# Kernel optimization log

Measured on AMD Instinct MI355X. Metric: run time of the kernel, lower is better.

Reference implementation:

```python
import jax, jax.numpy as jnp
import numpy as np
import math

B, S, D, H = 4, 1024, 1024, 16
HD = D // H
R = 128  # max_rel_pos
EPS = 1e-5

def setup_inputs() -> dict:
    key = jax.random.key(0)
    ks = jax.random.split(key, 20)
    sd = 1.0 / math.sqrt(D)
    def lin(k, din, dout):
        return jax.random.normal(k, (din, dout), jnp.float32) * (1.0 / math.sqrt(din))
    return {
        "x": jax.random.normal(ks[0], (B, S, D), jnp.float32),
        "wq": lin(ks[1], D, D), "bq": jnp.zeros((D,), jnp.float32),
        "wk": lin(ks[2], D, D), "bk": jnp.zeros((D,), jnp.float32),
        "wv": lin(ks[3], D, D), "bv": jnp.zeros((D,), jnp.float32),
        "wo": lin(ks[4], D, D), "bo": jnp.zeros((D,), jnp.float32),
        "rel_embed": jax.random.normal(ks[5], (2 * R + 1, HD), jnp.float32),
        "ln1_g": jnp.ones((D,), jnp.float32), "ln1_b": jnp.zeros((D,), jnp.float32),
        "ln2_g": jnp.ones((D,), jnp.float32), "ln2_b": jnp.zeros((D,), jnp.float32),
        "w1": lin(ks[6], D, 4 * D), "b1": jnp.zeros((4 * D,), jnp.float32),
        "w2": lin(ks[7], 4 * D, D), "b2": jnp.zeros((D,), jnp.float32),
    }

def _layernorm(x, g, b):
    mu = jnp.mean(x, axis=-1, keepdims=True)
    var = jnp.mean(jnp.square(x - mu), axis=-1, keepdims=True)
    return (x - mu) * jax.lax.rsqrt(var + EPS) * g + b

def _block(x, wq, bq, wk, bk, wv, bv, wo, bo, rel_embed,
           ln1_g, ln1_b, ln2_g, ln2_b, w1, b1, w2, b2):
    h = _layernorm(x, ln1_g, ln1_b)
    # project and split heads: [B,S,D] -> [B,H,S,HD]
    def heads(y):
        return y.reshape(B, S, H, HD).transpose(0, 2, 1, 3)
    Q = heads(h @ wq + bq)
    K = heads(h @ wk + bk)
    V = heads(h @ wv + bv)
    scale = 1.0 / math.sqrt(HD)
    scores = jnp.einsum("bhqd,bhkd->bhqk", Q, K) * scale
    # relative positions: clamp(q-k, -R, R) + R
    pos = jnp.arange(S)
    rel_idx = jnp.clip(pos[None, :] - pos[:, None], -R, R) + R  # [S,S]
    rel = rel_embed[rel_idx]  # [S,S,HD]
    scores = scores + jnp.einsum("bhqd,qkd->bhqk", Q, rel) * scale
    attn = jax.nn.softmax(scores, axis=-1)
    out = jnp.einsum("bhqk,bhkd->bhqd", attn, V)
    out = out.transpose(0, 2, 1, 3).reshape(B, S, D) @ wo + bo
    x = x + out  # dropout is identity in eval
    h2 = _layernorm(x, ln2_g, ln2_b)
    ff = jax.nn.gelu(h2 @ w1 + b1, approximate=False) @ w2 + b2
    return x + ff

def reference(x, wq, bq, wk, bk, wv, bv, wo, bo, rel_embed,
              ln1_g, ln1_b, ln2_g, ln2_b, w1, b1, w2, b2):
    return _block(x, wq, bq, wk, bk, wv, bv, wo, bo, rel_embed,
                  ln1_g, ln1_b, ln2_g, ln2_b, w1, b1, w2, b2)
```

## Files before the change

### kernel.cpp

```cpp
#include <hip/hip_runtime.h>

typedef unsigned short u16;
typedef __bf16 bf16x8 __attribute__((ext_vector_type(8)));
typedef float f32x4 __attribute__((ext_vector_type(4)));

#define QSCALE 0.18033688011112042f

__device__ __forceinline__ float b2f(u16 x) {
    unsigned int u = ((unsigned int)x) << 16;
    return __builtin_bit_cast(float, u);
}
__device__ __forceinline__ u16 f2bf(float f) {
    unsigned int u = __builtin_bit_cast(unsigned int, f);
    u += 0x7fffu + ((u >> 16) & 1u);
    return (u16)(u >> 16);
}
__device__ __forceinline__ void lds_load16(const u16* g, u16* l) {
    __builtin_amdgcn_global_load_lds(
        (const __attribute__((address_space(1))) void*)g,
        (__attribute__((address_space(3))) void*)l, 16, 0, 0);
}

__global__ void prep_kernel(
    const float* __restrict__ wq, const float* __restrict__ wk,
    const float* __restrict__ wv, const float* __restrict__ wo,
    const float* __restrict__ w1, const float* __restrict__ w2,
    const float* __restrict__ rel,
    const float* __restrict__ bq, const float* __restrict__ bk,
    const float* __restrict__ bv,
    u16* __restrict__ wqkvT, u16* __restrict__ woT,
    u16* __restrict__ w1T, u16* __restrict__ w2T,
    u16* __restrict__ relb, float* __restrict__ bqkv) {
    int bid = blockIdx.x;
    int tx = threadIdx.x, ty = threadIdx.y;
    if (bid < 12288) {
        __shared__ u16 tile[32][33];
        const float* in;
        u16* out;
        int R, C, bx, by;
        if (bid < 4096) {
            int z = bid >> 10, i = bid & 1023;
            in = (z == 0) ? wq : (z == 1) ? wk : (z == 2) ? wv : wo;
            out = (z < 3) ? wqkvT + (size_t)z * 1024 * 1024 : woT;
            R = 1024; C = 1024;
            bx = (i & 31) * 32; by = (i >> 5) * 32;
        } else if (bid < 8192) {
            int i = bid - 4096;
            in = w1; out = w1T; R = 1024; C = 4096;
            bx = (i & 127) * 32; by = (i >> 7) * 32;
        } else {
            int i = bid - 8192;
            in = w2; out = w2T; R = 4096; C = 1024;
            bx = (i & 31) * 32; by = (i >> 5) * 32;
        }
#pragma unroll
        for (int i = 0; i < 32; i += 8)
            tile[ty + i][tx] = f2bf(in[(size_t)(by + ty + i) * C + bx + tx]);
        __syncthreads();
#pragma unroll
        for (int i = 0; i < 32; i += 8)
            out[(size_t)(bx + ty + i) * R + by + tx] = tile[tx][ty + i];
    } else if (bid < 12353) {
        int i = (bid - 12288) * 256 + ty * 32 + tx;
        if (i < 257 * 64) relb[i] = f2bf(rel[i]);
    } else {
        int i = (bid - 12353) * 256 + ty * 32 + tx;
        if (i < 3072)
            bqkv[i] = (i < 1024) ? bq[i] : (i < 2048 ? bk[i - 1024] : bv[i - 2048]);
    }
}

__global__ void transpose_v(const u16* __restrict__ in, int ldin, int coloff,
                            u16* __restrict__ out) {
    __shared__ u16 tile[32][33];
    size_t zout = (size_t)blockIdx.z << 20;
    int bx = blockIdx.x * 32, by = blockIdx.y * 32;
    int tx = threadIdx.x, ty = threadIdx.y;
#pragma unroll
    for (int i = 0; i < 32; i += 8)
        tile[ty + i][tx] =
            in[(size_t)(blockIdx.z * 1024 + by + ty + i) * ldin + coloff + bx + tx];
    __syncthreads();
#pragma unroll
    for (int i = 0; i < 32; i += 8)
        out[zout + (size_t)(bx + ty + i) * 1024 + by + tx] = tile[tx][ty + i];
}

__global__ __launch_bounds__(256) void ln_kernel(
    const u16* __restrict__ inb, const float* __restrict__ inf,
    const float* __restrict__ g, const float* __restrict__ b,
    u16* __restrict__ out) {
    int row = blockIdx.x, t = threadIdx.x;
    size_t base = (size_t)row * 1024 + t * 4;
    float v[4];
    if (inf) {
        float4 f = *(const float4*)(inf + base);
        v[0] = f.x; v[1] = f.y; v[2] = f.z; v[3] = f.w;
    } else {
        uint2 u = *(const uint2*)(inb + base);
        v[0] = b2f((u16)(u.x & 0xffff)); v[1] = b2f((u16)(u.x >> 16));
        v[2] = b2f((u16)(u.y & 0xffff)); v[3] = b2f((u16)(u.y >> 16));
    }
    float s = v[0] + v[1] + v[2] + v[3];
    float q = v[0] * v[0] + v[1] * v[1] + v[2] * v[2] + v[3] * v[3];
#pragma unroll
    for (int m = 1; m < 64; m <<= 1) {
        s += __shfl_xor(s, m);
        q += __shfl_xor(q, m);
    }
    __shared__ float rs[4], rq[4];
    __shared__ float mu_s, rstd_s;
    int w = t >> 6, lane = t & 63;
    if (lane == 0) { rs[w] = s; rq[w] = q; }
    __syncthreads();
    if (t == 0) {
        float S = rs[0] + rs[1] + rs[2] + rs[3];
        float Q2 = rq[0] + rq[1] + rq[2] + rq[3];
        float mu = S * (1.0f / 1024.0f);
        float var = Q2 * (1.0f / 1024.0f) - mu * mu;
        mu_s = mu;
        rstd_s = rsqrtf(var + 1e-5f);
    }
    __syncthreads();
    float mu = mu_s, rstd = rstd_s;
    u16 o[4];
#pragma unroll
    for (int i = 0; i < 4; i++) {
        int col = t * 4 + i;
        o[i] = f2bf((v[i] - mu) * rstd * g[col] + b[col]);
    }
    uint2 pk;
    pk.x = (unsigned)o[0] | ((unsigned)o[1] << 16);
    pk.y = (unsigned)o[2] | ((unsigned)o[3] << 16);
    *(uint2*)(out + base) = pk;
}

__global__ __launch_bounds__(256) void gemm_bt64(
    const u16* __restrict__ A, int lda,
    const u16* __restrict__ Bt, int ldb,
    const float* __restrict__ bias,
    const float* __restrict__ resid_f32, const u16* __restrict__ resid_bf,
    u16* __restrict__ outb, float* __restrict__ outf, int ldc,
    int K, float oscale, int gelu) {
    constexpr int AU = 16, BU = 8, UPW = (AU + BU) / 4;
    __shared__ __align__(16) u16 As[2][128 * 64];
    __shared__ __align__(16) u16 Bs[2][64 * 64];
    int t = threadIdx.x, w = t >> 6, lane = t & 63;
    int m0 = blockIdx.y * 128, n0 = blockIdx.x * 64;
    int lo = lane & 15, hi = lane >> 4;
    int wr = w >> 1, wc = w & 1;
    f32x4 acc[4][2];
#pragma unroll
    for (int i = 0; i < 4; i++)
#pragma unroll
        for (int j = 0; j < 2; j++) acc[i][j] = (f32x4){0.f, 0.f, 0.f, 0.f};

    auto stage = [&](int k0, int buf) {
#pragma unroll
        for (int uu = 0; uu < UPW; ++uu) {
            int u = w * UPW + uu;
            if (u < AU) {
                int s = u * 64 + lane;
                int row = s >> 3, cg = (lane & 7) ^ (row & 7);
                lds_load16(A + (size_t)(m0 + row) * lda + k0 + cg * 8,
                           &As[buf][u * 512]);
            } else {
                int u2 = u - AU;
                int s = u2 * 64 + lane;
                int row = s >> 3, cg = (lane & 7) ^ (row & 7);
                lds_load16(Bt + (size_t)(n0 + row) * ldb + k0 + cg * 8,
                           &Bs[buf][u2 * 512]);
            }
        }
    };

    int nk = K >> 6;
    stage(0, 0);
    for (int kk = 0; kk < nk; ++kk) {
        __syncthreads();
        if (kk + 1 < nk) stage((kk + 1) << 6, (kk + 1) & 1);
        int buf = kk & 1;
#pragma unroll
        for (int k2 = 0; k2 < 2; ++k2) {
            bf16x8 a[4], bb[2];
#pragma unroll
            for (int i = 0; i < 4; i++) {
                int row = wr * 64 + i * 16 + lo;
                int g = (k2 * 4 + hi) ^ (row & 7);
                a[i] = *(const bf16x8*)&As[buf][row * 64 + g * 8];
            }
#pragma unroll
            for (int j = 0; j < 2; j++) {
                int row = wc * 32 + j * 16 + lo;
                int g = (k2 * 4 + hi) ^ (row & 7);
                bb[j] = *(const bf16x8*)&Bs[buf][row * 64 + g * 8];
            }
#pragma unroll
            for (int i = 0; i < 4; i++)
#pragma unroll
                for (int j = 0; j < 2; j++)
                    acc[i][j] = __builtin_amdgcn_mfma_f32_16x16x32_bf16(a[i], bb[j], acc[i][j], 0, 0, 0);
        }
    }
#pragma unroll
    for (int j = 0; j < 2; j++) {
        int col = n0 + wc * 32 + j * 16 + lo;
        float bv = bias ? bias[col] : 0.f;
#pragma unroll
        for (int i = 0; i < 4; i++) {
            int rbase = m0 + wr * 64 + i * 16 + hi * 4;
#pragma unroll
            for (int r = 0; r < 4; r++) {
                float v = fmaf(acc[i][j][r], oscale, bv);
                if (gelu) v = 0.5f * v * (1.f + erff(v * 0.70710678118654752f));
                size_t ridx = (size_t)(rbase + r) * ldc + col;
                if (resid_f32) v += resid_f32[ridx];
                if (resid_bf) v += b2f(resid_bf[ridx]);
                if (outf) outf[ridx] = v;
                if (outb) outb[ridx] = f2bf(v);
            }
        }
    }
}

__global__ __launch_bounds__(256) void gemm_bt128k64(
    const u16* __restrict__ A, int lda,
    const u16* __restrict__ Bt, int ldb,
    const float* __restrict__ bias, const u16* __restrict__ resid_bf,
    u16* __restrict__ outb, float* __restrict__ outf, int ldc,
    int K, float oscale, int gelu) {
    __shared__ __align__(16) u16 As[2][128 * 64];
    __shared__ __align__(16) u16 Bs[2][128 * 64];
    int t = threadIdx.x, w = t >> 6, lane = t & 63;
    int m0 = blockIdx.y * 128, n0 = blockIdx.x * 128;
    int lo = lane & 15, hi = lane >> 4;
    int wr = w >> 1, wc = w & 1;
    f32x4 acc[4][4];
#pragma unroll
    for (int i = 0; i < 4; i++)
#pragma unroll
        for (int j = 0; j < 4; j++) acc[i][j] = (f32x4){0.f, 0.f, 0.f, 0.f};

    auto stage = [&](int k0, int buf) {
#pragma unroll
        for (int uu = 0; uu < 4; ++uu) {
            int u = w * 4 + uu;
            int s = u * 64 + lane;
            int row = s >> 3, cg = (lane & 7) ^ (row & 7);
            lds_load16(A + (size_t)(m0 + row) * lda + k0 + cg * 8,
                       &As[buf][u * 512]);
        }
#pragma unroll
        for (int uu = 0; uu < 4; ++uu) {
            int u = w * 4 + uu;
            int s = u * 64 + lane;
            int row = s >> 3, cg = (lane & 7) ^ (row & 7);
            lds_load16(Bt + (size_t)(n0 + row) * ldb + k0 + cg * 8,
                       &Bs[buf][u * 512]);
        }
    };

    int nk = K >> 6;
    stage(0, 0);
    for (int kk = 0; kk < nk; ++kk) {
        __syncthreads();
        if (kk + 1 < nk) stage((kk + 1) << 6, (kk + 1) & 1);
        int buf = kk & 1;
#pragma unroll
        for (int k2 = 0; k2 < 2; ++k2) {
            bf16x8 a[4], bb[4];
#pragma unroll
            for (int i = 0; i < 4; i++) {
                int row = wr * 64 + i * 16 + lo;
                int g = (k2 * 4 + hi) ^ (row & 7);
                a[i] = *(const bf16x8*)&As[buf][row * 64 + g * 8];
            }
#pragma unroll
            for (int j = 0; j < 4; j++) {
                int row = wc * 64 + j * 16 + lo;
                int g = (k2 * 4 + hi) ^ (row & 7);
                bb[j] = *(const bf16x8*)&Bs[buf][row * 64 + g * 8];
            }
#pragma unroll
            for (int i = 0; i < 4; i++)
#pragma unroll
                for (int j = 0; j < 4; j++)
                    acc[i][j] = __builtin_amdgcn_mfma_f32_16x16x32_bf16(a[i], bb[j], acc[i][j], 0, 0, 0);
        }
    }
#pragma unroll
    for (int j = 0; j < 4; j++) {
        int col = n0 + wc * 64 + j * 16 + lo;
        float bv = bias ? bias[col] : 0.f;
#pragma unroll
        for (int i = 0; i < 4; i++) {
            int rbase = m0 + wr * 64 + i * 16 + hi * 4;
#pragma unroll
            for (int r = 0; r < 4; r++) {
                float v = fmaf(acc[i][j][r], oscale, bv);
                if (gelu) v = 0.5f * v * (1.f + erff(v * 0.70710678118654752f));
                size_t ridx = (size_t)(rbase + r) * ldc + col;
                if (resid_bf) v += b2f(resid_bf[ridx]);
                if (outf) outf[ridx] = v;
                if (outb) outb[ridx] = f2bf(v);
            }
        }
    }
}

__global__ __launch_bounds__(256) void attn_kernel(
    const u16* __restrict__ QKV, const u16* __restrict__ Vtg,
    const u16* __restrict__ relb, u16* __restrict__ Ob) {
    __shared__ __align__(16) u16 KsL[2][4096];
    __shared__ __align__(16) u16 VsL[2][4096];
    __shared__ __align__(16) u16 Ps[4][16 * 72];
    __shared__ __align__(16) u16 Rb[4][16 * 280];
    int t = threadIdx.x, w = t >> 6, lane = t & 63;
    int bid = blockIdx.x;
    int qblk = bid & 15, h = (bid >> 4) & 15, bb = bid >> 8;
    int lo = lane & 15, hi = lane >> 4;
    int q0b = qblk * 64;
    int q0 = q0b + w * 16;

    const u16* qrow = QKV + ((size_t)(bb * 1024 + q0 + lo) * 3072 + h * 64 + hi * 8);
    bf16x8 qf0 = *(const bf16x8*)qrow;
    bf16x8 qf1 = *(const bf16x8*)(qrow + 32);

    const u16* Kg = QKV + 1024 + ((size_t)(bb * 1024)) * 3072 + h * 64;
    const u16* Vg = Vtg + ((size_t)(bb * 1024 + h * 64)) * 1024;

    auto stage = [&](int k0, int buf) {
#pragma unroll
        for (int half = 0; half < 2; ++half) {
            int s = half * 256 + w * 64 + lane;
            int row = s >> 3, cg = (s & 7) ^ (row & 7);
            lds_load16(Kg + (size_t)(k0 + row) * 3072 + cg * 8,
                       &KsL[buf][(half * 256 + w * 64) * 8]);
            lds_load16(Vg + (size_t)row * 1024 + k0 + cg * 8,
                       &VsL[buf][(half * 256 + w * 64) * 8]);
        }
    };

    stage(0, 0);

#pragma unroll 4
    for (int pt = 0; pt < 17; ++pt) {
        bf16x8 rf0 = *(const bf16x8*)&relb[(pt * 16 + lo) * 64 + hi * 8];
        bf16x8 rf1 = *(const bf16x8*)&relb[(pt * 16 + lo) * 64 + 32 + hi * 8];
        f32x4 cz = (f32x4){0.f, 0.f, 0.f, 0.f};
        cz = __builtin_amdgcn_mfma_f32_16x16x32_bf16(qf0, rf0, cz, 0, 0, 0);
        cz = __builtin_amdgcn_mfma_f32_16x16x32_bf16(qf1, rf1, cz, 0, 0, 0);
#pragma unroll
        for (int r = 0; r < 4; r++)
            Rb[w][(hi * 4 + r) * 280 + pt * 16 + lo] =
                f2bf(fmaf(cz[r], QSCALE, -16.0f));
    }
    float blo[4], bhi[4];
#pragma unroll
    for (int r = 0; r < 4; r++) {
        blo[r] = b2f(Rb[w][(hi * 4 + r) * 280]);
        bhi[r] = b2f(Rb[w][(hi * 4 + r) * 280 + 256]);
    }

    f32x4 oacc[4];
#pragma unroll
    for (int j = 0; j < 4; j++) oacc[j] = (f32x4){0.f, 0.f, 0.f, 0.f};
    float l_[4] = {0.f, 0.f, 0.f, 0.f};

    for (int c = 0; c < 16; ++c) {
        int k0 = c * 64;
        __syncthreads();
        if (c < 15) stage(k0 + 64, (c + 1) & 1);
        const u16* Ksb = KsL[c & 1];
        const u16* Vsb = VsL[c & 1];

        f32x4 sc[4];
#pragma unroll
        for (int kt = 0; kt < 4; kt++) {
            int row = kt * 16 + lo, rx = row & 7;
            bf16x8 kf0 = *(const bf16x8*)&Ksb[(row * 8 + (hi ^ rx)) * 8];
            bf16x8 kf1 = *(const bf16x8*)&Ksb[(row * 8 + ((4 + hi) ^ rx)) * 8];
            f32x4 zz = (f32x4){0.f, 0.f, 0.f, 0.f};
            sc[kt] = __builtin_amdgcn_mfma_f32_16x16x32_bf16(qf0, kf0, zz, 0, 0, 0);
            sc[kt] = __builtin_amdgcn_mfma_f32_16x16x32_bf16(qf1, kf1, sc[kt], 0, 0, 0);
        }
        float bt[4][4];
        if (k0 + 192 <= q0b) {
#pragma unroll
            for (int kt = 0; kt < 4; kt++)
#pragma unroll
                for (int r = 0; r < 4; r++) bt[kt][r] = blo[r];
        } else if (k0 >= q0b + 192) {
#pragma unroll
            for (int kt = 0; kt < 4; kt++)
#pragma unroll
                for (int r = 0; r < 4; r++) bt[kt][r] = bhi[r];
        } else {
#pragma unroll
            for (int kt = 0; kt < 4; kt++)
#pragma unroll
                for (int r = 0; r < 4; r++) {
                    int lq = hi * 4 + r;
                    int p = (k0 + kt * 16 + lo) - (q0 + lq);
                    p = p < -128 ? -128 : (p > 128 ? 128 : p);
                    p += 128;
                    bt[kt][r] = b2f(Rb[w][lq * 280 + p]);
                }
        }
#pragma unroll
        for (int kt = 0; kt < 4; kt++)
#pragma unroll
            for (int r = 0; r < 4; r++) {
                float s = fmaf(sc[kt][r], QSCALE, bt[kt][r]);
                float p = __builtin_amdgcn_exp2f(s);
                l_[r] += p;
                Ps[w][(hi * 4 + r) * 72 + kt * 16 + lo] =
                    (u16)(__builtin_bit_cast(unsigned int, p) >> 16);
            }
        bf16x8 pf0 = *(const bf16x8*)&Ps[w][lo * 72 + 8 * hi];
        bf16x8 pf1 = *(const bf16x8*)&Ps[w][lo * 72 + 32 + 8 * hi];
#pragma unroll
        for (int j = 0; j < 4; j++) {
            int row = j * 16 + lo, rx = row & 7;
            bf16x8 vf0 = *(const bf16x8*)&Vsb[(row * 8 + (hi ^ rx)) * 8];
            bf16x8 vf1 = *(const bf16x8*)&Vsb[(row * 8 + ((4 + hi) ^ rx)) * 8];
            oacc[j] = __builtin_amdgcn_mfma_f32_16x16x32_bf16(pf0, vf0, oacc[j], 0, 0, 0);
            oacc[j] = __builtin_amdgcn_mfma_f32_16x16x32_bf16(pf1, vf1, oacc[j], 0, 0, 0);
        }
    }
#pragma unroll
    for (int r = 0; r < 4; r++) {
#pragma unroll
        for (int m = 1; m < 16; m <<= 1) l_[r] += __shfl_xor(l_[r], m);
    }
#pragma unroll
    for (int r = 0; r < 4; r++) {
        float inv = 1.f / l_[r];
        int q = q0 + hi * 4 + r;
#pragma unroll
        for (int j = 0; j < 4; j++)
            Ob[(size_t)(bb * 1024 + q) * 1024 + h * 64 + j * 16 + lo] =
                f2bf(oacc[j][r] * inv);
    }
}

extern "C" void kernel_launch(void* const* d_in, const int* in_sizes, int n_in,
                              void* d_out, int out_size, void* d_ws, size_t ws_size,
                              hipStream_t stream) {
    const float* x   = (const float*)d_in[0];
    const float* wq  = (const float*)d_in[1];
    const float* bq  = (const float*)d_in[2];
    const float* wk  = (const float*)d_in[3];
    const float* bk  = (const float*)d_in[4];
    const float* wv  = (const float*)d_in[5];
    const float* bv  = (const float*)d_in[6];
    const float* wo  = (const float*)d_in[7];
    const float* bo  = (const float*)d_in[8];
    const float* rel = (const float*)d_in[9];
    const float* g1  = (const float*)d_in[10];
    const float* be1 = (const float*)d_in[11];
    const float* g2  = (const float*)d_in[12];
    const float* be2 = (const float*)d_in[13];
    const float* w1  = (const float*)d_in[14];
    const float* bf1 = (const float*)d_in[15];
    const float* w2  = (const float*)d_in[16];
    const float* bf2 = (const float*)d_in[17];

    char* ws = (char*)d_ws;
    const size_t MB = 1024ull * 1024ull;
    u16* wqkvT = (u16*)(ws + 0 * MB);
    u16* woT  = (u16*)(ws + 6 * MB);
    u16* w1T  = (u16*)(ws + 8 * MB);
    u16* w2T  = (u16*)(ws + 16 * MB);
    u16* h    = (u16*)(ws + 24 * MB);
    u16* QKV  = (u16*)(ws + 32 * MB);
    u16* Vtg  = (u16*)(ws + 56 * MB);
    u16* x2b  = (u16*)(ws + 64 * MB);
    u16* att  = (u16*)(ws + 112 * MB);
    u16* relb = (u16*)(ws + 120 * MB);
    float* bqkv = (float*)(ws + 120 * MB + 128 * 1024);
    u16* ff1  = (u16*)(ws + 32 * MB);
    u16* h2   = h;

    dim3 tb(32, 8);
    prep_kernel<<<12365, tb, 0, stream>>>(wq, wk, wv, wo, w1, w2, rel,
                                          bq, bk, bv,
                                          wqkvT, woT, w1T, w2T, relb, bqkv);

    ln_kernel<<<4096, 256, 0, stream>>>(nullptr, x, g1, be1, h);

    gemm_bt128k64<<<dim3(24, 32), 256, 0, stream>>>(h, 1024, wqkvT, 1024,
        bqkv, nullptr, QKV, nullptr, 3072, 1024, 1.f, 0);
    transpose_v<<<dim3(32, 32, 4), tb, 0, stream>>>(QKV, 3072, 2048, Vtg);

    attn_kernel<<<1024, 256, 0, stream>>>(QKV, Vtg, relb, att);

    gemm_bt64<<<dim3(16, 32), 256, 0, stream>>>(att, 1024, woT, 1024,
        bo, x, nullptr, x2b, nullptr, 1024, 1024, 1.f, 0);

    ln_kernel<<<4096, 256, 0, stream>>>(x2b, nullptr, g2, be2, h2);

    gemm_bt128k64<<<dim3(32, 32), 256, 0, stream>>>(h2, 1024, w1T, 1024,
        bf1, nullptr, ff1, nullptr, 4096, 1024, 1.f, 1);
    gemm_bt64<<<dim3(16, 32), 256, 0, stream>>>(ff1, 4096, w2T, 4096,
        bf2, nullptr, x2b, nullptr, (float*)d_out, 1024, 4096, 1.f, 0);
}
```

Before: 395.6 us.

## Fuse V transpose into QKV GEMM epilogue and LN1 into prep kernel

After: 392.3 us. Within noise of the previous version (-0.8%).

```diff
diff --git a/kernel.cpp b/kernel.cpp
--- a/kernel.cpp
+++ b/kernel.cpp
@@ -28,11 +28,14 @@
     const float* __restrict__ rel,
     const float* __restrict__ bq, const float* __restrict__ bk,
     const float* __restrict__ bv,
+    const float* __restrict__ x, const float* __restrict__ g1,
+    const float* __restrict__ be1,
     u16* __restrict__ wqkvT, u16* __restrict__ woT,
     u16* __restrict__ w1T, u16* __restrict__ w2T,
-    u16* __restrict__ relb, float* __restrict__ bqkv) {
+    u16* __restrict__ relb, float* __restrict__ bqkv, u16* __restrict__ h) {
     int bid = blockIdx.x;
     int tx = threadIdx.x, ty = threadIdx.y;
+    int t = ty * 32 + tx;
     if (bid < 12288) {
         __shared__ u16 tile[32][33];
         const float* in;
@@ -61,46 +64,61 @@
         for (int i = 0; i < 32; i += 8)
             out[(size_t)(bx + ty + i) * R + by + tx] = tile[tx][ty + i];
     } else if (bid < 12353) {
-        int i = (bid - 12288) * 256 + ty * 32 + tx;
+        int i = (bid - 12288) * 256 + t;
         if (i < 257 * 64) relb[i] = f2bf(rel[i]);
-    } else {
-        int i = (bid - 12353) * 256 + ty * 32 + tx;
+    } else if (bid < 12365) {
+        int i = (bid - 12353) * 256 + t;
         if (i < 3072)
             bqkv[i] = (i < 1024) ? bq[i] : (i < 2048 ? bk[i - 1024] : bv[i - 2048]);
-    }
-}
-
-__global__ void transpose_v(const u16* __restrict__ in, int ldin, int coloff,
-                            u16* __restrict__ out) {
-    __shared__ u16 tile[32][33];
-    size_t zout = (size_t)blockIdx.z << 20;
-    int bx = blockIdx.x * 32, by = blockIdx.y * 32;
-    int tx = threadIdx.x, ty = threadIdx.y;
-#pragma unroll
-    for (int i = 0; i < 32; i += 8)
-        tile[ty + i][tx] =
-            in[(size_t)(blockIdx.z * 1024 + by + ty + i) * ldin + coloff + bx + tx];
-    __syncthreads();
-#pragma unroll
-    for (int i = 0; i < 32; i += 8)
-        out[zout + (size_t)(bx + ty + i) * 1024 + by + tx] = tile[tx][ty + i];
+    } else {
+        int row = bid - 12365;
+        size_t base = (size_t)row * 1024 + t * 4;
+        float4 f = *(const float4*)(x + base);
+        float v[4] = {f.x, f.y, f.z, f.w};
+        float s = v[0] + v[1] + v[2] + v[3];
+        float q = v[0] * v[0] + v[1] * v[1] + v[2] * v[2] + v[3] * v[3];
+#pragma unroll
+        for (int m = 1; m < 64; m <<= 1) {
+            s += __shfl_xor(s, m);
+            q += __shfl_xor(q, m);
+        }
+        __shared__ float rs[4], rq[4];
+        __shared__ float mu_s, rstd_s;
+        int w = t >> 6, lane = t & 63;
+        if (lane == 0) { rs[w] = s; rq[w] = q; }
+        __syncthreads();
+        if (t == 0) {
+            float S = rs[0] + rs[1] + rs[2] + rs[3];
+            float Q2 = rq[0] + rq[1] + rq[2] + rq[3];
+            float mu = S * (1.0f / 1024.0f);
+            float var = Q2 * (1.0f / 1024.0f) - mu * mu;
+            mu_s = mu;
+            rstd_s = rsqrtf(var + 1e-5f);
+        }
+        __syncthreads();
+        float mu = mu_s, rstd = rstd_s;
+        u16 o[4];
+#pragma unroll
+        for (int i = 0; i < 4; i++) {
+            int col = t * 4 + i;
+            o[i] = f2bf((v[i] - mu) * rstd * g1[col] + be1[col]);
+        }
+        uint2 pk;
+        pk.x = (unsigned)o[0] | ((unsigned)o[1] << 16);
+        pk.y = (unsigned)o[2] | ((unsigned)o[3] << 16);
+        *(uint2*)(h + base) = pk;
+    }
 }
 
 __global__ __launch_bounds__(256) void ln_kernel(
-    const u16* __restrict__ inb, const float* __restrict__ inf,
-    const float* __restrict__ g, const float* __restrict__ b,
-    u16* __restrict__ out) {
+    const u16* __restrict__ inb, const float* __restrict__ g,
+    const float* __restrict__ b, u16* __restrict__ out) {
     int row = blockIdx.x, t = threadIdx.x;
     size_t base = (size_t)row * 1024 + t * 4;
     float v[4];
-    if (inf) {
-        float4 f = *(const float4*)(inf + base);
-        v[0] = f.x; v[1] = f.y; v[2] = f.z; v[3] = f.w;
-    } else {
-        uint2 u = *(const uint2*)(inb + base);
-        v[0] = b2f((u16)(u.x & 0xffff)); v[1] = b2f((u16)(u.x >> 16));
-        v[2] = b2f((u16)(u.y & 0xffff)); v[3] = b2f((u16)(u.y >> 16));
-    }
+    uint2 u = *(const uint2*)(inb + base);
+    v[0] = b2f((u16)(u.x & 0xffff)); v[1] = b2f((u16)(u.x >> 16));
+    v[2] = b2f((u16)(u.y & 0xffff)); v[3] = b2f((u16)(u.y >> 16));
     float s = v[0] + v[1] + v[2] + v[3];
     float q = v[0] * v[0] + v[1] * v[1] + v[2] * v[2] + v[3] * v[3];
 #pragma unroll
@@ -228,7 +246,7 @@
     const u16* __restrict__ Bt, int ldb,
     const float* __restrict__ bias, const u16* __restrict__ resid_bf,
     u16* __restrict__ outb, float* __restrict__ outf, int ldc,
-    int K, float oscale, int gelu) {
+    int K, float oscale, int gelu, u16* __restrict__ vtg) {
     __shared__ __align__(16) u16 As[2][128 * 64];
     __shared__ __align__(16) u16 Bs[2][128 * 64];
     int t = threadIdx.x, w = t >> 6, lane = t & 63;
@@ -287,6 +305,38 @@
                 for (int j = 0; j < 4; j++)
                     acc[i][j] = __builtin_amdgcn_mfma_f32_16x16x32_bf16(a[i], bb[j], acc[i][j], 0, 0, 0);
         }
+    }
+    if (vtg && n0 >= 2048) {
+        __syncthreads();
+        u16* TT = &As[0][0];
+#pragma unroll
+        for (int j = 0; j < 4; j++) {
+            int coll = wc * 64 + j * 16 + lo;
+            int colg = n0 + coll;
+            float bv = bias ? bias[colg] : 0.f;
+            int sw = (coll & 15) << 3;
+#pragma unroll
+            for (int i = 0; i < 4; i++) {
+                int ml = wr * 64 + i * 16 + hi * 4;
+                u16 pk[4];
+#pragma unroll
+                for (int r = 0; r < 4; r++) pk[r] = f2bf(acc[i][j][r] + bv);
+                *(unsigned long long*)&TT[coll * 128 + (ml ^ sw)] =
+                    *(unsigned long long*)pk;
+            }
+        }
+        __syncthreads();
+        int bb2 = m0 >> 10, s0 = m0 & 1023;
+        size_t zout = (size_t)bb2 << 20;
+#pragma unroll
+        for (int pass = 0; pass < 8; ++pass) {
+            int idx = pass * 256 + t;
+            int drow = idx >> 4, mc = (idx & 15) * 8;
+            int sw = (drow & 15) << 3;
+            uint4 v4 = *(uint4*)&TT[drow * 128 + (mc ^ sw)];
+            *(uint4*)&vtg[zout + (size_t)(n0 - 2048 + drow) * 1024 + s0 + mc] = v4;
+        }
+        return;
     }
 #pragma unroll
     for (int j = 0; j < 4; j++) {
@@ -483,25 +533,22 @@
     u16* h2   = h;
 
     dim3 tb(32, 8);
-    prep_kernel<<<12365, tb, 0, stream>>>(wq, wk, wv, wo, w1, w2, rel,
-                                          bq, bk, bv,
-                                          wqkvT, woT, w1T, w2T, relb, bqkv);
-
-    ln_kernel<<<4096, 256, 0, stream>>>(nullptr, x, g1, be1, h);
+    prep_kernel<<<16461, tb, 0, stream>>>(wq, wk, wv, wo, w1, w2, rel,
+                                          bq, bk, bv, x, g1, be1,
+                                          wqkvT, woT, w1T, w2T, relb, bqkv, h);
 
     gemm_bt128k64<<<dim3(24, 32), 256, 0, stream>>>(h, 1024, wqkvT, 1024,
-        bqkv, nullptr, QKV, nullptr, 3072, 1024, 1.f, 0);
-    transpose_v<<<dim3(32, 32, 4), tb, 0, stream>>>(QKV, 3072, 2048, Vtg);
+        bqkv, nullptr, QKV, nullptr, 3072, 1024, 1.f, 0, Vtg);
 
     attn_kernel<<<1024, 256, 0, stream>>>(QKV, Vtg, relb, att);
 
     gemm_bt64<<<dim3(16, 32), 256, 0, stream>>>(att, 1024, woT, 1024,
         bo, x, nullptr, x2b, nullptr, 1024, 1024, 1.f, 0);
 
-    ln_kernel<<<4096, 256, 0, stream>>>(x2b, nullptr, g2, be2, h2);
+    ln_kernel<<<4096, 256, 0, stream>>>(x2b, g2, be2, h2);
 
     gemm_bt128k64<<<dim3(32, 32), 256, 0, stream>>>(h2, 1024, w1T, 1024,
-        bf1, nullptr, ff1, nullptr, 4096, 1024, 1.f, 1);
+        bf1, nullptr, ff1, nullptr, 4096, 1024, 1.f, 1, nullptr);
     gemm_bt64<<<dim3(16, 32), 256, 0, stream>>>(ff1, 4096, w2T, 4096,
         bf2, nullptr, x2b, nullptr, (float*)d_out, 1024, 4096, 1.f, 0);
 }
```
